# Optimization experiments

Hardware: AMD Instinct MI355X
Metric: run time of the kernel (lower is better)

The kernel has to match this reference:

```python
import jax, jax.numpy as jnp
import numpy as np

STRIDE = 16
H = 100
W = 100
C = 1024
A = 9  # anchors per location
IOU_THRESH = 0.7
MIN_SIZE = 16.0


def _conv2d(x, w, b):
    # x: [N,C,H,W], w: [O,I,kh,kw] (torch OIHW), 'same' padding, stride 1
    y = jax.lax.conv_general_dilated(
        x, w, window_strides=(1, 1), padding='SAME',
        dimension_numbers=('NCHW', 'OIHW', 'NCHW'))
    return y + b[None, :, None, None]


def _nms_keep(boxes, valid, iou_thresh):
    # boxes: [N,4] (y1,x1,y2,x2) sorted by descending score; valid: [N] bool
    n = boxes.shape[0]
    y1, x1, y2, x2 = boxes[:, 0], boxes[:, 1], boxes[:, 2], boxes[:, 3]
    areas = (y2 - y1) * (x2 - x1)
    idx = jnp.arange(n)

    def body(i, keep):
        iy1 = jnp.maximum(y1[i], y1)
        ix1 = jnp.maximum(x1[i], x1)
        iy2 = jnp.minimum(y2[i], y2)
        ix2 = jnp.minimum(x2[i], x2)
        inter = jnp.maximum(iy2 - iy1, 0.0) * jnp.maximum(ix2 - ix1, 0.0)
        iou = inter / (areas[i] + areas - inter + 1e-8)
        suppress = (iou > iou_thresh) & (idx > i)
        return jnp.where(keep[i], keep & ~suppress, keep)

    return jax.lax.fori_loop(0, n, body, valid)


def _make_anchor_map():
    ratios = np.array([0.5, 1.0, 2.0])
    sizes = np.array([128.0, 256.0, 512.0])
    ah = (sizes[:, None] * np.sqrt(ratios)[None, :]).reshape(-1)  # [9]
    aw = (sizes[:, None] / np.sqrt(ratios)[None, :]).reshape(-1)  # [9]
    cy = (np.arange(H) + 0.5) * STRIDE
    cx = (np.arange(W) + 0.5) * STRIDE
    am = np.zeros((H, W, A, 4), dtype=np.float32)
    am[..., 0] = cy[:, None, None]
    am[..., 1] = cx[None, :, None]
    am[..., 2] = ah[None, None, :]
    am[..., 3] = aw[None, None, :]
    return jnp.asarray(am.reshape(H, W, A * 4))


def setup_inputs() -> dict:
    key = jax.random.key(0)
    ks = jax.random.split(key, 4)
    feature_map = jax.random.normal(ks[0], (1, C, H, W), jnp.float32)
    # module init: normal(0, 0.01) weights, zero biases
    w1 = jax.random.normal(ks[1], (C, C, 3, 3), jnp.float32) * 0.01
    b1 = jnp.zeros((C,), jnp.float32)
    w_cls = jax.random.normal(ks[2], (A, C, 1, 1), jnp.float32) * 0.01
    b_cls = jnp.zeros((A,), jnp.float32)
    w_box = jax.random.normal(ks[3], (A * 4, C, 1, 1), jnp.float32) * 0.01
    b_box = jnp.zeros((A * 4,), jnp.float32)
    return {
        'feature_map': feature_map,
        'image_shape': jnp.array([3, H * STRIDE, W * STRIDE], jnp.int32),
        'anchor_map': _make_anchor_map(),
        'anchor_valid_map': jnp.ones((H, W, A), jnp.int32),
        'max_proposals_pre_nms': 6000,
        'max_proposals_post_nms': 300,
        'w1': w1, 'b1': b1,
        'w_cls': w_cls, 'b_cls': b_cls,
        'w_box': w_box, 'b_box': b_box,
    }


def reference(feature_map, image_shape, anchor_map, anchor_valid_map,
              max_proposals_pre_nms, max_proposals_post_nms,
              w1, b1, w_cls, b_cls, w_box, b_box):
    pre = int(max_proposals_pre_nms)
    post = int(max_proposals_post_nms)

    y = jax.nn.relu(_conv2d(feature_map, w1, b1))
    objectness_score_map = jax.nn.sigmoid(_conv2d(y, w_cls, b_cls))  # [1,9,H,W]
    box_deltas_map = _conv2d(y, w_box, b_box)                        # [1,36,H,W]
    # NCHW -> NHWC, like permute(0,2,3,1)
    objectness_score_map = jnp.transpose(objectness_score_map, (0, 2, 3, 1))
    box_deltas_map = jnp.transpose(box_deltas_map, (0, 2, 3, 1))

    h, w, a = anchor_valid_map.shape
    n = h * w * a
    anchors = anchor_map.reshape(n, 4)                # (cy, cx, ah, aw)
    scores = objectness_score_map.reshape(n)
    deltas = jax.lax.stop_gradient(box_deltas_map.reshape(n, 4))  # .detach()
    # allow_edge_proposals=True -> no valid filtering

    # decode (means=0, stds=1): center = c + t*s, size = s*exp(t)
    center = anchors[:, 0:2] + deltas[:, 0:2] * anchors[:, 2:4]
    size = anchors[:, 2:4] * jnp.exp(deltas[:, 2:4])
    proposals = jnp.concatenate([center - 0.5 * size, center + 0.5 * size], axis=1)

    # argsort ascending then flip == descending (matches torch code)
    order = jnp.argsort(scores)[::-1][:pre]
    proposals = proposals[order]
    scores_sorted = scores[order]

    # clip to image
    y1x1 = jnp.maximum(proposals[:, 0:2], 0.0)
    y2 = jnp.minimum(proposals[:, 2], image_shape[1].astype(proposals.dtype))
    x2 = jnp.minimum(proposals[:, 3], image_shape[2].astype(proposals.dtype))
    proposals = jnp.concatenate([y1x1, y2[:, None], x2[:, None]], axis=1)

    height = proposals[:, 2] - proposals[:, 0]
    width = proposals[:, 3] - proposals[:, 1]
    valid = (height >= MIN_SIZE) & (width >= MIN_SIZE)

    keep = _nms_keep(proposals, valid, IOU_THRESH)

    # fixed-shape selection of first `post` kept boxes (score-ordered)
    pos = jnp.where(keep, jnp.arange(pre), pre)
    pos = jnp.sort(pos)[:post]
    ok = pos < pre
    safe = jnp.minimum(pos, pre - 1)
    out_proposals = jnp.where(ok[:, None], proposals[safe], 0.0)  # [post,4]

    return objectness_score_map, box_deltas_map, out_proposals
```

## Files before the change

kernel.cpp:

```cpp
#include <hip/hip_runtime.h>
#include <hip/hip_fp16.h>
#include <stdint.h>

#define HH 100
#define WW 100
#define NPIX 10000
#define CIN 1024
#define COUT 1024
#define NA 9
#define NANCH 90000
#define PRE 6000
#define POST 300
#define SORTN 131072
#define MASKW 96
#define NW 94
#define K9 9216
#define SPAD 10404
#define WSCALE 1024.0f
#define KH 48

#define PXT 160
#define BUFB 53248
#define NSTEP 288

#define HEADB 157

typedef unsigned short u16;
typedef _Float16 f16x8 __attribute__((ext_vector_type(8)));
typedef float f32x4 __attribute__((ext_vector_type(4)));

__device__ __forceinline__ void gload16(const u16* g, char* l)
{
    __builtin_amdgcn_global_load_lds((const void*)g, (void*)l, 16, 0, 0);
}

__global__ __launch_bounds__(256) void xsplit(
    const float* __restrict__ x, u16* __restrict__ xt1, u16* __restrict__ xt2)
{
    __shared__ unsigned sh[32][257];
    const int t = threadIdx.x;
    if (blockIdx.x >= 313) {
        int idx = (blockIdx.x - 313) * 4 + blockIdx.y;
        int spx;
        if (idx < 102) spx = idx;
        else if (idx < 204) spx = 10302 + (idx - 102);
        else { int k = idx - 204; spx = (1 + (k >> 1)) * 102 + (k & 1) * 101; }
        size_t o = (size_t)spx * 1024 + t * 4;
        *(ushort4*)&xt1[o] = make_ushort4(0, 0, 0, 0);
        *(ushort4*)&xt2[o] = make_ushort4(0, 0, 0, 0);
        return;
    }
    const int px0 = blockIdx.x * 32;
    const int ci0 = blockIdx.y * 256;
    for (int it = 0; it < 32; ++it) {
        int idx = it * 256 + t;
        int a = idx >> 5, b = idx & 31;
        int p = px0 + b;
        float v = (p < NPIX) ? x[(size_t)(ci0 + a) * NPIX + p] : 0.f;
        __half h1 = __float2half_rn(v);
        __half h2 = __float2half_rn(v - __half2float(h1));
        sh[b][a] = ((unsigned)__half_as_ushort(h1) << 16) | __half_as_ushort(h2);
    }
    __syncthreads();
    for (int it = 0; it < 8; ++it) {
        int u = it * 256 + t;
        int pl = u >> 6, cq = u & 63;
        int p = px0 + pl;
        if (p >= NPIX) continue;
        int r = p / 100, c = p - r * 100;
        int spx = (r + 1) * 102 + (c + 1);
        unsigned w0 = sh[pl][cq * 4 + 0], w1 = sh[pl][cq * 4 + 1];
        unsigned w2 = sh[pl][cq * 4 + 2], w3 = sh[pl][cq * 4 + 3];
        ushort4 v1 = make_ushort4((u16)(w0 >> 16), (u16)(w1 >> 16), (u16)(w2 >> 16), (u16)(w3 >> 16));
        ushort4 v2 = make_ushort4((u16)(w0 & 0xffff), (u16)(w1 & 0xffff), (u16)(w2 & 0xffff), (u16)(w3 & 0xffff));
        size_t o = (size_t)spx * 1024 + ci0 + cq * 4;
        *(ushort4*)&xt1[o] = v1;
        *(ushort4*)&xt2[o] = v2;
    }
}

__global__ __launch_bounds__(256) void wsplit(
    const float* __restrict__ w1, u16* __restrict__ wp1, u16* __restrict__ wp2,
    const float* __restrict__ wcls, const float* __restrict__ wbox,
    float* __restrict__ wh)
{
    __shared__ float sw[K9];
    const int t = threadIdx.x;
    if (blockIdx.x >= COUT) {
        int e = (blockIdx.x - COUT) * 256 + t;
        if (e < CIN * KH) {
            int c = e / KH, k = e - c * KH;
            float v = 0.f;
            if (k < 9) v = wcls[k * CIN + c];
            else if (k < 45) v = wbox[(k - 9) * CIN + c];
            wh[e] = v;
        }
        return;
    }
    const int co = blockIdx.x;
    for (int it = 0; it < 36; ++it)
        sw[it * 256 + t] = w1[(size_t)co * K9 + it * 256 + t];
    __syncthreads();
    for (int tap = 0; tap < 9; ++tap) {
        for (int it = 0; it < 4; ++it) {
            int ci = it * 256 + t;
            float v = sw[ci * 9 + tap] * WSCALE;
            __half h1 = __float2half_rn(v);
            __half h2 = __float2half_rn(v - __half2float(h1));
            size_t o = (size_t)tap * (COUT * 1024) + (size_t)co * 1024 + ci;
            wp1[o] = __half_as_ushort(h1);
            wp2[o] = __half_as_ushort(h2);
        }
    }
}

__global__ __launch_bounds__(512, 1) void conv_mfma(
    const u16* __restrict__ xt1, const u16* __restrict__ xt2,
    const u16* __restrict__ wp1, const u16* __restrict__ wp2,
    const float* __restrict__ b1, float* __restrict__ y)
{
    __shared__ __align__(16) char lds[3 * BUFB];
    const int t = threadIdx.x;
    const int co0 = blockIdx.x * 256;
    const int px0 = blockIdx.y * PXT;
    const int lane = t & 63;
    const int wv = __builtin_amdgcn_readfirstlane(t >> 6);
    const int wm = (wv >> 1) * 64;
    const int wn = (wv & 1) * 80;

    const int qs = (lane & 3) ^ ((lane >> 3) & 3);

    const int ar0 = wv * 32, ar1 = wv * 32 + 16;
    const size_t aOff0 = (size_t)(co0 + ar0 + (lane >> 2)) * 1024 + qs * 8;
    const size_t aOff1 = (size_t)(co0 + ar1 + (lane >> 2)) * 1024 + qs * 8;

    const int nbu = (wv < 2) ? 2 : 1;
    size_t bOff[2]; int bLds[2];
#pragma unroll
    for (int s = 0; s < 2; ++s) {
        int r0 = (wv + 8 * s) * 16;
        if (r0 >= PXT) r0 = 0;
        int p = px0 + r0 + (lane >> 2);
        if (p > NPIX - 1) p = NPIX - 1;
        int rr = p / 100, cc = p - rr * 100;
        bOff[s] = (size_t)((rr + 1) * 102 + cc + 1) * 1024 + qs * 8;
        bLds[s] = r0 * 64;
    }

    const int qf = ((lane >> 4) ^ (((lane & 15) >> 1) & 3)) * 16;
    const int fA = (wm + (lane & 15)) * 64 + qf;
    const int fB = 32768 + (wn + (lane & 15)) * 64 + qf;

    f32x4 acc[4][5] = {};

    auto STAGE = [&](int buf, int step) {
        char* lb = lds + buf * BUFB;
        const int tap = step >> 5;
        const int ci0 = (step & 31) << 5;
        const int dy = (tap * 11) >> 5;
        const int tsh = (dy - 1) * 102 + (tap - dy * 3) - 1;
        const size_t adelta = (size_t)tap * 1048576 + ci0;
        const ptrdiff_t bdelta = (ptrdiff_t)tsh * 1024 + ci0;
        gload16(wp1 + aOff0 + adelta, lb + ar0 * 64);
        gload16(wp1 + aOff1 + adelta, lb + ar1 * 64);
        gload16(wp2 + aOff0 + adelta, lb + 16384 + ar0 * 64);
        gload16(wp2 + aOff1 + adelta, lb + 16384 + ar1 * 64);
#pragma unroll
        for (int s = 0; s < 2; ++s) {
            if (s < nbu) {
                gload16(xt1 + (ptrdiff_t)bOff[s] + bdelta, lb + 32768 + bLds[s]);
                gload16(xt2 + (ptrdiff_t)bOff[s] + bdelta, lb + 43008 + bLds[s]);
            }
        }
    };

    auto COMPUTE = [&](int buf) {
        const char* lb = lds + buf * BUFB;
        f16x8 A1[4], A2[4], B1[5], B2[5];
#pragma unroll
        for (int mi = 0; mi < 4; ++mi) {
            A1[mi] = *(const f16x8*)(lb + fA + mi * 1024);
            A2[mi] = *(const f16x8*)(lb + 16384 + fA + mi * 1024);
        }
#pragma unroll
        for (int ni = 0; ni < 5; ++ni) {
            B1[ni] = *(const f16x8*)(lb + fB + ni * 1024);
            B2[ni] = *(const f16x8*)(lb + fB + 10240 + ni * 1024);
        }
#pragma unroll
        for (int mi = 0; mi < 4; ++mi)
#pragma unroll
            for (int ni = 0; ni < 5; ++ni) {
                acc[mi][ni] = __builtin_amdgcn_mfma_f32_16x16x32_f16(A1[mi], B1[ni], acc[mi][ni], 0, 0, 0);
                acc[mi][ni] = __builtin_amdgcn_mfma_f32_16x16x32_f16(A1[mi], B2[ni], acc[mi][ni], 0, 0, 0);
                acc[mi][ni] = __builtin_amdgcn_mfma_f32_16x16x32_f16(A2[mi], B1[ni], acc[mi][ni], 0, 0, 0);
            }
    };

    STAGE(0, 0);
    STAGE(1, 1);
    asm volatile("s_waitcnt vmcnt(6)" ::: "memory");
    __builtin_amdgcn_s_barrier();

    int cb = 0;
    for (int k = 0; k < NSTEP; ++k) {
        int sb = cb + 2; if (sb >= 3) sb -= 3;
        if (k + 2 < NSTEP) STAGE(sb, k + 2);
        COMPUTE(cb);
        if (k >= NSTEP - 2) {
            asm volatile("s_waitcnt vmcnt(0)" ::: "memory");
        } else {
            asm volatile("s_waitcnt vmcnt(6)" ::: "memory");
        }
        __builtin_amdgcn_s_barrier();
        if (++cb == 3) cb = 0;
    }

    const int q4 = (lane >> 4) * 4, nl = lane & 15;
    const float inv = 1.0f / WSCALE;
#pragma unroll
    for (int mi = 0; mi < 4; ++mi) {
        const int cob = co0 + wm + mi * 16 + q4;
        const float bb0 = b1[cob + 0], bb1 = b1[cob + 1];
        const float bb2 = b1[cob + 2], bb3 = b1[cob + 3];
#pragma unroll
        for (int ni = 0; ni < 5; ++ni) {
            const int px = px0 + wn + ni * 16 + nl;
            if (px < NPIX) {
                y[(size_t)(cob + 0) * NPIX + px] = fmaxf(acc[mi][ni][0] * inv + bb0, 0.f);
                y[(size_t)(cob + 1) * NPIX + px] = fmaxf(acc[mi][ni][1] * inv + bb1, 0.f);
                y[(size_t)(cob + 2) * NPIX + px] = fmaxf(acc[mi][ni][2] * inv + bb2, 0.f);
                y[(size_t)(cob + 3) * NPIX + px] = fmaxf(acc[mi][ni][3] * inv + bb3, 0.f);
            }
        }
    }
}

__global__ __launch_bounds__(256) void rpn_head(
    const float* __restrict__ y, const float* __restrict__ wh,
    const float* __restrict__ bcls, const float* __restrict__ bbox,
    const float* __restrict__ am, const int* __restrict__ ishape,
    float* __restrict__ out_scores, float* __restrict__ out_deltas,
    float4* __restrict__ boxes, unsigned long long* __restrict__ keys)
{
    __shared__ float red[4][64][KH + 1];
    const int t = threadIdx.x;
    if (blockIdx.x >= HEADB) {
        int i = NANCH + (blockIdx.x - HEADB) * 256 + t;
        if (i < SORTN) keys[i] = 0ull;
        return;
    }
    const int lane = t & 63;
    const int q = __builtin_amdgcn_readfirstlane(t >> 6);
    const int p = blockIdx.x * 64 + lane;
    const int pp = (p < NPIX) ? p : (NPIX - 1);

    float acc[45];
#pragma unroll
    for (int k = 0; k < 45; ++k) acc[k] = 0.f;

    const float* __restrict__ yq  = y  + (size_t)q * 256 * NPIX + pp;
    const float* __restrict__ whq = wh + (size_t)q * 256 * KH;
    for (int c = 0; c < 256; ++c) {
        float yv = yq[(size_t)c * NPIX];
        const float* wr = whq + c * KH;
#pragma unroll
        for (int k = 0; k < 45; ++k) acc[k] += yv * wr[k];
    }

#pragma unroll
    for (int k = 0; k < 45; ++k) red[q][lane][k] = acc[k];
    __syncthreads();

    if (t >= 64 || p >= NPIX) return;

    float s[45];
#pragma unroll
    for (int k = 0; k < 45; ++k)
        s[k] = (red[0][lane][k] + red[1][lane][k]) + (red[2][lane][k] + red[3][lane][k]);

    const float imh = (float)ishape[1], imw = (float)ishape[2];
#pragma unroll
    for (int a = 0; a < 9; ++a) {
        const int i = p * NA + a;
        float logit = s[a] + bcls[a];
        float score = 1.f / (1.f + expf(-logit));
        float d0 = s[9 + a * 4 + 0] + bbox[a * 4 + 0];
        float d1 = s[9 + a * 4 + 1] + bbox[a * 4 + 1];
        float d2 = s[9 + a * 4 + 2] + bbox[a * 4 + 2];
        float d3 = s[9 + a * 4 + 3] + bbox[a * 4 + 3];
        out_scores[i] = score;
        out_deltas[i * 4 + 0] = d0;
        out_deltas[i * 4 + 1] = d1;
        out_deltas[i * 4 + 2] = d2;
        out_deltas[i * 4 + 3] = d3;

        float cy = am[i * 4 + 0], cx = am[i * 4 + 1];
        float ah = am[i * 4 + 2], aw = am[i * 4 + 3];
        float ctry = cy + d0 * ah, ctrx = cx + d1 * aw;
        float hh = ah * expf(d2), ww = aw * expf(d3);
        float y1 = fmaxf(ctry - 0.5f * hh, 0.f);
        float x1 = fmaxf(ctrx - 0.5f * ww, 0.f);
        float y2 = fminf(ctry + 0.5f * hh, imh);
        float x2 = fminf(ctrx + 0.5f * ww, imw);
        boxes[i] = make_float4(y1, x1, y2, x2);
        unsigned sb = __float_as_uint(score);
        keys[i] = ((unsigned long long)sb << 32) | (unsigned)i;
    }
}

__global__ __launch_bounds__(1024) void bitonic_local8k(unsigned long long* keys)
{
    __shared__ unsigned long long s[8192];
    const int base = blockIdx.x * 8192, t = threadIdx.x;
    for (int k = t; k < 8192; k += 1024) s[k] = keys[base + k];
    for (int L = 2; L <= 8192; L <<= 1) {
        for (int d = L >> 1; d >= 1; d >>= 1) {
            __syncthreads();
            for (int pr = t; pr < 4096; pr += 1024) {
                int i = ((pr & ~(d - 1)) << 1) | (pr & (d - 1));
                int j = i + d;
                bool desc = (((base + i) & L) == 0);
                unsigned long long va = s[i], vb = s[j];
                bool sw = desc ? (va < vb) : (va > vb);
                if (sw) { s[i] = vb; s[j] = va; }
            }
        }
    }
    __syncthreads();
    for (int k = t; k < 8192; k += 1024) keys[base + k] = s[k];
}

__global__ __launch_bounds__(256) void bitonic_gpass(unsigned long long* keys, int L, int d)
{
    int pr = blockIdx.x * 256 + threadIdx.x;
    int i = ((pr & ~(d - 1)) << 1) | (pr & (d - 1));
    int j = i + d;
    bool desc = ((i & L) == 0);
    unsigned long long va = keys[i], vb = keys[j];
    bool sw = desc ? (va < vb) : (va > vb);
    if (sw) { keys[i] = vb; keys[j] = va; }
}

__global__ __launch_bounds__(1024) void bitonic_lmerge8k(
    unsigned long long* keys, int L,
    const float4* __restrict__ boxes, float4* __restrict__ box_s,
    unsigned long long* __restrict__ validw)
{
    __shared__ unsigned long long s[8192];
    const int base = blockIdx.x * 8192, t = threadIdx.x;
    for (int k = t; k < 8192; k += 1024) s[k] = keys[base + k];
    const bool desc = ((base & L) == 0);
    for (int d = 4096; d >= 1; d >>= 1) {
        __syncthreads();
        for (int pr = t; pr < 4096; pr += 1024) {
            int i = ((pr & ~(d - 1)) << 1) | (pr & (d - 1));
            int j = i + d;
            unsigned long long va = s[i], vb = s[j];
            bool sw = desc ? (va < vb) : (va > vb);
            if (sw) { s[i] = vb; s[j] = va; }
        }
    }
    __syncthreads();
    for (int k = t; k < 8192; k += 1024) keys[base + k] = s[k];
    if (L == SORTN && blockIdx.x == 0) {
        for (int k = t; k < 6144; k += 1024) {
            bool valid = false;
            if (k < PRE) {
                unsigned idx = (unsigned)(s[k] & 0xffffffffull);
                float4 b = boxes[idx];
                box_s[k] = b;
                valid = ((b.z - b.x) >= 16.f) && ((b.w - b.y) >= 16.f);
            }
            unsigned long long bal = __ballot(valid);
            if ((t & 63) == 0) validw[k >> 6] = bal;
        }
    }
}

__global__ __launch_bounds__(128) void nms_mask(
    const float4* __restrict__ box_s, unsigned long long* __restrict__ mask)
{
    const int i = blockIdx.x;
    const int w = threadIdx.x;
    if (w >= NW) return;
    float4 bi = box_s[i];
    float areai = (bi.z - bi.x) * (bi.w - bi.y);
    unsigned long long m = 0ull;
    const int j0 = w * 64;
    if (j0 + 63 > i) {
#pragma unroll 4
        for (int b = 0; b < 64; ++b) {
            int j = j0 + b;
            if (j <= i || j >= PRE) continue;
            float4 bj = box_s[j];
            float areaj = (bj.z - bj.x) * (bj.w - bj.y);
            float iy1 = fmaxf(bi.x, bj.x), ix1 = fmaxf(bi.y, bj.y);
            float iy2 = fminf(bi.z, bj.z), ix2 = fminf(bi.w, bj.w);
            float inter = fmaxf(iy2 - iy1, 0.f) * fmaxf(ix2 - ix1, 0.f);
            float iou = inter / (areai + areaj - inter + 1e-8f);
            if (iou > 0.7f) m |= (1ull << b);
        }
    }
    mask[(size_t)i * MASKW + w] = m;
}

__global__ __launch_bounds__(256) void nms_scan_out(
    const unsigned long long* __restrict__ mask,
    const unsigned long long* __restrict__ validw,
    const float4* __restrict__ box_s, float* __restrict__ outp)
{
    __shared__ unsigned long long kw_s[NW];
    __shared__ int prefix[NW];
    const int t = threadIdx.x;
    if (t < 64) {
        const int l = t;
        unsigned long long r0 = ~validw[l];
        unsigned long long r1 = (l < NW - 64) ? ~validw[64 + l] : ~0ull;
        unsigned long long p0[16], p1[16];
#pragma unroll
        for (int k = 0; k < 16; ++k) {
            p0[k] = mask[(size_t)k * MASKW + l];
            p1[k] = (l < NW - 64) ? mask[(size_t)k * MASKW + 64 + l] : 0ull;
        }
        int kept = 0;
        for (int w = 0; w < NW && kept < POST; ++w) {
            unsigned long long Wc = (w < 64) ? __shfl(r0, w) : __shfl(r1, w - 64);
#pragma unroll 16
            for (int b = 0; b < 64; ++b) {
                int i = w * 64 + b;
                if (i >= PRE) break;
                int slot = i & 15;
                unsigned long long m0 = p0[slot], m1 = p1[slot];
                int nxt = i + 16;
                if (nxt < PRE) {
                    p0[slot] = mask[(size_t)nxt * MASKW + l];
                    p1[slot] = (l < NW - 64) ? mask[(size_t)nxt * MASKW + 64 + l] : 0ull;
                }
                if (!((Wc >> b) & 1ull)) {
                    r0 |= m0; r1 |= m1;
                    Wc = (w < 64) ? __shfl(r0, w) : __shfl(r1, w - 64);
                    ++kept;
                }
            }
        }
        kw_s[l] = ~r0;
        if (l < NW - 64) kw_s[64 + l] = ~r1;
    }
    __syncthreads();
    if (t == 0) {
        int cum = 0;
        for (int w = 0; w < NW; ++w) { prefix[w] = cum; cum += __popcll(kw_s[w]); }
    }
    for (int k = t; k < POST * 4; k += 256) outp[k] = 0.f;
    __syncthreads();
    for (int i = t; i < PRE; i += 256) {
        int w = i >> 6, b = i & 63;
        unsigned long long kw = kw_s[w];
        if ((kw >> b) & 1ull) {
            int rank = prefix[w] + __popcll(kw & ((1ull << b) - 1ull));
            if (rank < POST) {
                float4 bx = box_s[i];
                outp[rank * 4 + 0] = bx.x;
                outp[rank * 4 + 1] = bx.y;
                outp[rank * 4 + 2] = bx.z;
                outp[rank * 4 + 3] = bx.w;
            }
        }
    }
}

extern "C" void kernel_launch(void* const* d_in, const int* in_sizes, int n_in,
                              void* d_out, int out_size, void* d_ws, size_t ws_size,
                              hipStream_t stream)
{
    const float* x      = (const float*)d_in[0];
    const int*   ishape = (const int*)  d_in[1];
    const float* am     = (const float*)d_in[2];
    const float* w1   = (const float*)d_in[6];
    const float* b1   = (const float*)d_in[7];
    const float* wcls = (const float*)d_in[8];
    const float* bcls = (const float*)d_in[9];
    const float* wbox = (const float*)d_in[10];
    const float* bbox = (const float*)d_in[11];
    float* out = (float*)d_out;

    char* ws = (char*)d_ws;
    size_t off = 0;
    float* y  = (float*)(ws + off);  off += (size_t)COUT * NPIX * 4;
    u16* xt1  = (u16*)(ws + off);    off += (size_t)SPAD * 1024 * 2;
    u16* xt2  = (u16*)(ws + off);    off += (size_t)SPAD * 1024 * 2;
    u16* wp1  = (u16*)(ws + off);    off += (size_t)9 * COUT * 1024 * 2;
    u16* wp2  = (u16*)(ws + off);    off += (size_t)9 * COUT * 1024 * 2;
    float4* boxes = (float4*)(ws + off);              off += (size_t)NANCH * 16;
    unsigned long long* keys = (unsigned long long*)(ws + off); off += (size_t)SORTN * 8;
    float4* box_s = (float4*)(ws + off);              off += (size_t)PRE * 16;
    unsigned long long* validw = (unsigned long long*)(ws + off); off += 96 * 8;
    unsigned long long* maskb  = (unsigned long long*)(ws + off); off += (size_t)PRE * MASKW * 8;
    float* wh = (float*)(ws + off);  off += (size_t)CIN * KH * 4;

    xsplit<<<dim3(414, 4), 256, 0, stream>>>(x, xt1, xt2);
    wsplit<<<COUT + (CIN * KH + 255) / 256, 256, 0, stream>>>(w1, wp1, wp2, wcls, wbox, wh);
    conv_mfma<<<dim3(4, (NPIX + PXT - 1) / PXT), 512, 0, stream>>>(xt1, xt2, wp1, wp2, b1, y);
    rpn_head<<<HEADB + (SORTN - NANCH + 255) / 256, 256, 0, stream>>>(
        y, wh, bcls, bbox, am, ishape, out, out + NANCH, boxes, keys);
    bitonic_local8k<<<SORTN / 8192, 1024, 0, stream>>>(keys);
    for (int L = 16384; L <= SORTN; L <<= 1) {
        for (int d = L >> 1; d >= 8192; d >>= 1)
            bitonic_gpass<<<SORTN / 512, 256, 0, stream>>>(keys, L, d);
        bitonic_lmerge8k<<<SORTN / 8192, 1024, 0, stream>>>(keys, L, boxes, box_s, validw);
    }
    nms_mask<<<PRE, 128, 0, stream>>>(box_s, maskb);
    nms_scan_out<<<1, 256, 0, stream>>>(maskb, validw, box_s, out + (size_t)NANCH * 5);
}
```

Baseline: 1.082 ms.

## Unroll conv pipeline by three, raise MFMA priority, and sort in 16K shared tiles

The conv main loop is unrolled by the three-buffer rotation so buffer indices become compile-time constants. It also adds s_setprio around the MFMA compute and uses per-wave vmcnt wait counts. Separately, the bitonic sort's shared-memory tiles grow from 8K to 16K keys (128 KB of LDS), which cuts the number of global merge passes and kernel launches. The trade-off is fewer, larger sort blocks that each run 1024 threads and lower GPU occupancy, and any mismatch between the wait counts and the real number of outstanding loads could cause data hazards.

```diff
diff --git a/kernel.cpp b/kernel.cpp
--- a/kernel.cpp
+++ b/kernel.cpp
@@ -197,23 +197,36 @@
             }
     };
 
+    auto WAITC = [&]() {
+        if (wv < 2) asm volatile("s_waitcnt vmcnt(8)" ::: "memory");
+        else        asm volatile("s_waitcnt vmcnt(6)" ::: "memory");
+    };
+    auto WAIT0 = [&]() { asm volatile("s_waitcnt vmcnt(0)" ::: "memory"); };
+
     STAGE(0, 0);
     STAGE(1, 1);
-    asm volatile("s_waitcnt vmcnt(6)" ::: "memory");
+    WAITC();
     __builtin_amdgcn_s_barrier();
 
-    int cb = 0;
-    for (int k = 0; k < NSTEP; ++k) {
-        int sb = cb + 2; if (sb >= 3) sb -= 3;
-        if (k + 2 < NSTEP) STAGE(sb, k + 2);
-        COMPUTE(cb);
-        if (k >= NSTEP - 2) {
-            asm volatile("s_waitcnt vmcnt(0)" ::: "memory");
-        } else {
-            asm volatile("s_waitcnt vmcnt(6)" ::: "memory");
-        }
+    for (int k = 0; k < NSTEP; k += 3) {
+        if (k + 2 < NSTEP) STAGE(2, k + 2);
+        __builtin_amdgcn_s_setprio(1);
+        COMPUTE(0);
+        __builtin_amdgcn_s_setprio(0);
+        if (k >= NSTEP - 2) WAIT0(); else WAITC();
         __builtin_amdgcn_s_barrier();
-        if (++cb == 3) cb = 0;
+        if (k + 3 < NSTEP) STAGE(0, k + 3);
+        __builtin_amdgcn_s_setprio(1);
+        COMPUTE(1);
+        __builtin_amdgcn_s_setprio(0);
+        if (k + 1 >= NSTEP - 2) WAIT0(); else WAITC();
+        __builtin_amdgcn_s_barrier();
+        if (k + 4 < NSTEP) STAGE(1, k + 4);
+        __builtin_amdgcn_s_setprio(1);
+        COMPUTE(2);
+        __builtin_amdgcn_s_setprio(0);
+        if (k + 2 >= NSTEP - 2) WAIT0(); else WAITC();
+        __builtin_amdgcn_s_barrier();
     }
 
     const int q4 = (lane >> 4) * 4, nl = lane & 15;
@@ -309,15 +322,15 @@
     }
 }
 
-__global__ __launch_bounds__(1024) void bitonic_local8k(unsigned long long* keys)
-{
-    __shared__ unsigned long long s[8192];
-    const int base = blockIdx.x * 8192, t = threadIdx.x;
-    for (int k = t; k < 8192; k += 1024) s[k] = keys[base + k];
-    for (int L = 2; L <= 8192; L <<= 1) {
+__global__ __launch_bounds__(1024) void bitonic_local16k(unsigned long long* keys)
+{
+    __shared__ unsigned long long s[16384];
+    const int base = blockIdx.x * 16384, t = threadIdx.x;
+    for (int k = t; k < 16384; k += 1024) s[k] = keys[base + k];
+    for (int L = 2; L <= 16384; L <<= 1) {
         for (int d = L >> 1; d >= 1; d >>= 1) {
             __syncthreads();
-            for (int pr = t; pr < 4096; pr += 1024) {
+            for (int pr = t; pr < 8192; pr += 1024) {
                 int i = ((pr & ~(d - 1)) << 1) | (pr & (d - 1));
                 int j = i + d;
                 bool desc = (((base + i) & L) == 0);
@@ -328,7 +341,7 @@
         }
     }
     __syncthreads();
-    for (int k = t; k < 8192; k += 1024) keys[base + k] = s[k];
+    for (int k = t; k < 16384; k += 1024) keys[base + k] = s[k];
 }
 
 __global__ __launch_bounds__(256) void bitonic_gpass(unsigned long long* keys, int L, int d)
@@ -342,18 +355,18 @@
     if (sw) { keys[i] = vb; keys[j] = va; }
 }
 
-__global__ __launch_bounds__(1024) void bitonic_lmerge8k(
+__global__ __launch_bounds__(1024) void bitonic_lmerge16k(
     unsigned long long* keys, int L,
     const float4* __restrict__ boxes, float4* __restrict__ box_s,
     unsigned long long* __restrict__ validw)
 {
-    __shared__ unsigned long long s[8192];
-    const int base = blockIdx.x * 8192, t = threadIdx.x;
-    for (int k = t; k < 8192; k += 1024) s[k] = keys[base + k];
+    __shared__ unsigned long long s[16384];
+    const int base = blockIdx.x * 16384, t = threadIdx.x;
+    for (int k = t; k < 16384; k += 1024) s[k] = keys[base + k];
     const bool desc = ((base & L) == 0);
-    for (int d = 4096; d >= 1; d >>= 1) {
+    for (int d = 8192; d >= 1; d >>= 1) {
         __syncthreads();
-        for (int pr = t; pr < 4096; pr += 1024) {
+        for (int pr = t; pr < 8192; pr += 1024) {
             int i = ((pr & ~(d - 1)) << 1) | (pr & (d - 1));
             int j = i + d;
             unsigned long long va = s[i], vb = s[j];
@@ -362,7 +375,7 @@
         }
     }
     __syncthreads();
-    for (int k = t; k < 8192; k += 1024) keys[base + k] = s[k];
+    for (int k = t; k < 16384; k += 1024) keys[base + k] = s[k];
     if (L == SORTN && blockIdx.x == 0) {
         for (int k = t; k < 6144; k += 1024) {
             bool valid = false;
@@ -504,11 +517,11 @@
     conv_mfma<<<dim3(4, (NPIX + PXT - 1) / PXT), 512, 0, stream>>>(xt1, xt2, wp1, wp2, b1, y);
     rpn_head<<<HEADB + (SORTN - NANCH + 255) / 256, 256, 0, stream>>>(
         y, wh, bcls, bbox, am, ishape, out, out + NANCH, boxes, keys);
-    bitonic_local8k<<<SORTN / 8192, 1024, 0, stream>>>(keys);
-    for (int L = 16384; L <= SORTN; L <<= 1) {
-        for (int d = L >> 1; d >= 8192; d >>= 1)
+    bitonic_local16k<<<SORTN / 16384, 1024, 0, stream>>>(keys);
+    for (int L = 32768; L <= SORTN; L <<= 1) {
+        for (int d = L >> 1; d >= 16384; d >>= 1)
             bitonic_gpass<<<SORTN / 512, 256, 0, stream>>>(keys, L, d);
-        bitonic_lmerge8k<<<SORTN / 8192, 1024, 0, stream>>>(keys, L, boxes, box_s, validw);
+        bitonic_lmerge16k<<<SORTN / 16384, 1024, 0, stream>>>(keys, L, boxes, box_s, validw);
     }
     nms_mask<<<PRE, 128, 0, stream>>>(box_s, maskb);
     nms_scan_out<<<1, 256, 0, stream>>>(maskb, validw, box_s, out + (size_t)NANCH * 5);
```

Result: slower. 1.199 ms (+10.8%).
